# Performance work log

Hardware: AMD Instinct MI355X
Metric: run time of the kernel (lower is better)

## Reference

```python
import jax, jax.numpy as jnp
import numpy as np

B, S, HID = 2, 2048, 3072
H, HKV, D = 16, 8, 256
ROPE_THETA = 10000.0
NEG_INF = -1e9


def setup_inputs() -> dict:
    key = jax.random.key(0)
    ks = jax.random.split(key, 5)
    hidden_states = jax.random.normal(ks[0], (B, S, HID), jnp.float32)
    # rotary frequencies: complex freqs_cis = cos + i*sin, shape (B, S, D//2)
    inv_freq = 1.0 / (ROPE_THETA ** (np.arange(0, D, 2, dtype=np.float32) / D))
    ang = np.arange(S, dtype=np.float32)[:, None] * inv_freq[None, :]  # (S, D//2)
    cos = jnp.asarray(np.broadcast_to(np.cos(ang)[None], (B, S, D // 2)).copy())
    sin = jnp.asarray(np.broadcast_to(np.sin(ang)[None], (B, S, D // 2)).copy())
    causal = jnp.tril(jnp.ones((S, S), dtype=bool))
    mask = jnp.where(causal, 0.0, NEG_INF).astype(jnp.float32)[None, None]  # (1,1,S,S)
    wq = jax.random.normal(ks[1], (HID, H * D), jnp.float32) * 0.02
    wk = jax.random.normal(ks[2], (HID, HKV * D), jnp.float32) * 0.02
    wv = jax.random.normal(ks[3], (HID, HKV * D), jnp.float32) * 0.02
    wo = jax.random.normal(ks[4], (H * D, HID), jnp.float32) * 0.02
    return {"hidden_states": hidden_states, "cos": cos, "sin": sin, "mask": mask,
            "wq": wq, "wk": wk, "wv": wv, "wo": wo}


def _apply_rotary(x, cos, sin):
    # x: (B, S, Hx, D). Torch code forms complex pairs (x[..., :D/2], x[..., D/2:])
    # and multiplies by freqs_cis = cos + i*sin, then re-concats real||imag halves.
    half = x.shape[-1] // 2
    x1, x2 = x[..., :half], x[..., half:]
    c = cos[:, :, None, :]  # (B, S, 1, D/2)
    s = sin[:, :, None, :]
    return jnp.concatenate([x1 * c - x2 * s, x1 * s + x2 * c], axis=-1)


def reference(hidden_states, cos, sin, mask, wq, wk, wv, wo):
    b, s, _ = hidden_states.shape
    q = (hidden_states @ wq).reshape(b, s, H, D)
    k = (hidden_states @ wk).reshape(b, s, HKV, D)
    v = (hidden_states @ wv).reshape(b, s, HKV, D)
    q = _apply_rotary(q, cos, sin)
    k = _apply_rotary(k, cos, sin)
    # GQA: group query heads per kv head instead of materializing repeated K/V
    g = H // HKV
    qg = q.reshape(b, s, HKV, g, D)
    scaling = D ** (-0.5)
    scores = jnp.einsum('bskgd,btkd->bkgst', qg, k) * scaling  # (B,HKV,G,S,S)
    scores = scores + mask[:, :, None]  # broadcast (1,1,1,S,S)
    probs = jax.nn.softmax(scores, axis=-1)
    out = jnp.einsum('bkgst,btkd->bskgd', probs, v).reshape(b, s, H * D)
    return out @ wo
```

## Files before the change

### kernel.cpp

```cpp
#include <hip/hip_runtime.h>

typedef short bf16x8 __attribute__((ext_vector_type(8)));
typedef float f32x4 __attribute__((ext_vector_type(4)));

#define S_LEN 2048
#define NHQ 16
#define NKV 8
#define HD 256

__device__ __forceinline__ unsigned short f2bf(float f){
  unsigned u = __float_as_uint(f);
  unsigned r = (u + 0x7FFFu + ((u >> 16) & 1u)) >> 16;
  return (unsigned short)r;
}
__device__ __forceinline__ float bf2f(unsigned short h){
  return __uint_as_float(((unsigned)h) << 16);
}
__device__ __forceinline__ unsigned pack2(float a, float b){
  return (unsigned)f2bf(a) | ((unsigned)f2bf(b) << 16);
}

__global__ void k_conv(const float* __restrict__ in, unsigned short* __restrict__ out, int n){
  int i = (blockIdx.x * 256 + threadIdx.x) * 4;
  if (i < n){
    float4 v = *(const float4*)&in[i];
    ushort4 o;
    o.x = f2bf(v.x); o.y = f2bf(v.y); o.z = f2bf(v.z); o.w = f2bf(v.w);
    *(ushort4*)&out[i] = o;
  }
}

__global__ void k_tconv(const float* __restrict__ in, unsigned short* __restrict__ out, int R, int C){
  __shared__ float tile[32][33];
  int c0 = blockIdx.x * 32, r0 = blockIdx.y * 32;
  int tx = threadIdx.x, ty = threadIdx.y;
  for (int i = 0; i < 4; i++)
    tile[ty + i*8][tx] = in[(size_t)(r0 + ty + i*8) * C + c0 + tx];
  __syncthreads();
  for (int i = 0; i < 4; i++)
    out[(size_t)(c0 + ty + i*8) * R + r0 + tx] = f2bf(tile[tx][ty + i*8]);
}

__global__ void k_vtrans(const unsigned short* __restrict__ V, unsigned short* __restrict__ VT){
  __shared__ unsigned short tile[32][40];
  int s0 = blockIdx.x * 32, d0 = blockIdx.y * 32, bz = blockIdx.z;
  int b = bz >> 3, kv = bz & 7;
  int tx = threadIdx.x, ty = threadIdx.y;
  for (int i = 0; i < 4; i++)
    tile[ty + i*8][tx] = V[(size_t)(b * S_LEN + s0 + ty + i*8) * (NKV*HD) + kv*HD + d0 + tx];
  __syncthreads();
  for (int i = 0; i < 4; i++)
    VT[((size_t)(bz * HD + d0 + ty + i*8)) * S_LEN + s0 + tx] = tile[tx][ty + i*8];
}

__global__ void k_rope(unsigned short* buf, const float* __restrict__ cosb,
                       const float* __restrict__ sinb, int lgnh){
  int idx = blockIdx.x * 256 + threadIdx.x;
  int d = idx & 127;
  int h = (idx >> 7) & ((1 << lgnh) - 1);
  int t = idx >> (7 + lgnh);
  float c = cosb[t * 128 + d], s = sinb[t * 128 + d];
  size_t base = ((size_t)t << (lgnh + 8)) + ((size_t)h << 8) + d;
  float x1 = bf2f(buf[base]), x2 = bf2f(buf[base + 128]);
  buf[base]       = f2bf(x1 * c - x2 * s);
  buf[base + 128] = f2bf(x1 * s + x2 * c);
}

__global__ __launch_bounds__(256) void k_gemm_bt(const unsigned short* __restrict__ A,
    const unsigned short* __restrict__ Bt, void* __restrict__ Cp,
    int M, int N, int K, int out_bf16){
  __shared__ __align__(16) unsigned short smem[2 * 128 * 64];
  unsigned short* As = smem;
  unsigned short* Bs = smem + 128 * 64;
  int tid = threadIdx.x;
  int lane = tid & 63, wave = tid >> 6, quad = lane >> 4, l16 = lane & 15;
  int wm = wave >> 1, wn = wave & 1;
  int bm0 = blockIdx.y * 128, bn0 = blockIdx.x * 128;
  f32x4 acc[4][4] = {};
  for (int k0 = 0; k0 < K; k0 += 64){
    __syncthreads();
    for (int it = 0; it < 4; it++){
      int slot = it * 256 + tid;
      int row = slot >> 3, c = slot & 7;
      int pc = c ^ (row & 7);
      *(uint4*)&As[row * 64 + pc * 8] = *(const uint4*)&A[(size_t)(bm0 + row) * K + k0 + c * 8];
      *(uint4*)&Bs[row * 64 + pc * 8] = *(const uint4*)&Bt[(size_t)(bn0 + row) * K + k0 + c * 8];
    }
    __syncthreads();
    for (int ks = 0; ks < 2; ks++){
      bf16x8 af[4], bfr[4];
      for (int mt = 0; mt < 4; mt++){
        int row = wm * 64 + mt * 16 + l16;
        int pc = (ks * 4 + quad) ^ (row & 7);
        af[mt] = *(const bf16x8*)&As[row * 64 + pc * 8];
      }
      for (int nt = 0; nt < 4; nt++){
        int row = wn * 64 + nt * 16 + l16;
        int pc = (ks * 4 + quad) ^ (row & 7);
        bfr[nt] = *(const bf16x8*)&Bs[row * 64 + pc * 8];
      }
      for (int mt = 0; mt < 4; mt++)
        for (int nt = 0; nt < 4; nt++)
          acc[mt][nt] = __builtin_amdgcn_mfma_f32_16x16x32_bf16(af[mt], bfr[nt], acc[mt][nt], 0, 0, 0);
    }
  }
  float* Ct = (float*)smem;
  for (int p = 0; p < 2; p++){
    __syncthreads();
    if (wm == p){
      for (int mt = 0; mt < 4; mt++)
        for (int nt = 0; nt < 4; nt++)
          for (int r = 0; r < 4; r++)
            Ct[(mt * 16 + quad * 4 + r) * 128 + wn * 64 + nt * 16 + l16] = acc[mt][nt][r];
    }
    __syncthreads();
    if (out_bf16){
      unsigned short* O = (unsigned short*)Cp;
      for (int j = 0; j < 4; j++){
        int chunk = j * 256 + tid;
        int row = chunk >> 4, col = (chunk & 15) * 8;
        const float* src = &Ct[row * 128 + col];
        uint4 o;
        o.x = pack2(src[0], src[1]);
        o.y = pack2(src[2], src[3]);
        o.z = pack2(src[4], src[5]);
        o.w = pack2(src[6], src[7]);
        *(uint4*)&O[(size_t)(bm0 + p * 64 + row) * N + bn0 + col] = o;
      }
    } else {
      float* O = (float*)Cp;
      for (int j = 0; j < 8; j++){
        int chunk = j * 256 + tid;
        int row = chunk >> 5, col = (chunk & 31) * 4;
        *(float4*)&O[(size_t)(bm0 + p * 64 + row) * N + bn0 + col] = *(const float4*)&Ct[row * 128 + col];
      }
    }
  }
}

__global__ __launch_bounds__(256) void k_flash(const unsigned short* __restrict__ Q,
    const unsigned short* __restrict__ Kg, const unsigned short* __restrict__ VTg,
    unsigned short* __restrict__ Og){
  __shared__ __align__(16) unsigned short smem[32 * 264 + 256 * 40 + 4 * 16 * 40];
  unsigned short* Ks  = smem;
  unsigned short* VTs = smem + 32 * 264;
  unsigned short* Ps  = VTs + 256 * 40;
  int tid = threadIdx.x;
  int lane = tid & 63, wave = tid >> 6, quad = lane >> 4, l16 = lane & 15;
  int qt = blockIdx.x, hd_ = blockIdx.y;
  int b = hd_ >> 4, h = hd_ & 15, kv = h >> 1;

  bf16x8 qf[8];
  {
    size_t qoff = ((size_t)(b * S_LEN + qt * 64 + wave * 16 + l16)) * (NHQ * HD) + (size_t)h * HD;
    for (int ks = 0; ks < 8; ks++)
      qf[ks] = *(const bf16x8*)&Q[qoff + ks * 32 + quad * 8];
  }
  f32x4 acc[16] = {};
  float mrow[4], lrow[4];
  for (int r = 0; r < 4; r++){ mrow[r] = -1e30f; lrow[r] = 0.f; }
  int qmin = qt * 64 + wave * 16;
  int nkt = qt * 2 + 2;
  const float L2E = 1.4426950408889634f;
  const float scale = 0.0625f;

  for (int kt = 0; kt < nkt; kt++){
    __syncthreads();
    for (int it = 0; it < 4; it++){
      int slot = it * 256 + tid;
      int kr = slot >> 5, c = slot & 31;
      *(uint4*)&Ks[kr * 264 + c * 8] =
          *(const uint4*)&Kg[(size_t)(b * S_LEN + kt * 32 + kr) * (NKV*HD) + (size_t)kv * HD + c * 8];
      int dd = slot >> 2, c2 = slot & 3;
      *(uint4*)&VTs[dd * 40 + c2 * 8] =
          *(const uint4*)&VTg[((size_t)((b * NKV + kv) * HD + dd)) * S_LEN + kt * 32 + c2 * 8];
    }
    __syncthreads();
    if (kt * 32 > qmin + 15) continue;

    f32x4 sv[2] = {};
    for (int ks = 0; ks < 8; ks++){
      for (int nt = 0; nt < 2; nt++){
        bf16x8 kf = *(const bf16x8*)&Ks[(nt * 16 + l16) * 264 + ks * 32 + quad * 8];
        sv[nt] = __builtin_amdgcn_mfma_f32_16x16x32_bf16(qf[ks], kf, sv[nt], 0, 0, 0);
      }
    }
    float pv[2][4], tmax[4];
    for (int r = 0; r < 4; r++){
      int qr = qmin + quad * 4 + r;
      float mx = -1e30f;
      for (int nt = 0; nt < 2; nt++){
        int key = kt * 32 + nt * 16 + l16;
        float v = sv[nt][r] * scale;
        if (key > qr) v = -1e30f;
        pv[nt][r] = v;
        mx = fmaxf(mx, v);
      }
      tmax[r] = mx;
    }
    for (int off = 1; off < 16; off <<= 1)
      for (int r = 0; r < 4; r++)
        tmax[r] = fmaxf(tmax[r], __shfl_xor(tmax[r], off, 64));
    float alpha[4];
    for (int r = 0; r < 4; r++){
      float mn = fmaxf(mrow[r], tmax[r]);
      alpha[r] = exp2f((mrow[r] - mn) * L2E);
      mrow[r] = mn;
    }
    float pb[2][4], psum[4] = {0.f, 0.f, 0.f, 0.f};
    for (int nt = 0; nt < 2; nt++)
      for (int r = 0; r < 4; r++){
        float p = exp2f((pv[nt][r] - mrow[r]) * L2E);
        pb[nt][r] = p; psum[r] += p;
      }
    for (int off = 1; off < 16; off <<= 1)
      for (int r = 0; r < 4; r++)
        psum[r] += __shfl_xor(psum[r], off, 64);
    for (int r = 0; r < 4; r++) lrow[r] = lrow[r] * alpha[r] + psum[r];
    for (int i = 0; i < 16; i++)
      for (int r = 0; r < 4; r++) acc[i][r] *= alpha[r];
    int pbase = wave * 16 * 40;
    for (int nt = 0; nt < 2; nt++)
      for (int r = 0; r < 4; r++)
        Ps[pbase + (quad * 4 + r) * 40 + nt * 16 + l16] = f2bf(pb[nt][r]);
    bf16x8 pa = *(const bf16x8*)&Ps[pbase + l16 * 40 + quad * 8];
    for (int nt = 0; nt < 16; nt++){
      bf16x8 vf = *(const bf16x8*)&VTs[(nt * 16 + l16) * 40 + quad * 8];
      acc[nt] = __builtin_amdgcn_mfma_f32_16x16x32_bf16(pa, vf, acc[nt], 0, 0, 0);
    }
  }
  float inv[4];
  for (int r = 0; r < 4; r++) inv[r] = 1.0f / lrow[r];
  __syncthreads();
  unsigned short* Ot = smem + wave * 16 * 256;
  for (int nt = 0; nt < 16; nt++)
    for (int r = 0; r < 4; r++)
      Ot[(quad * 4 + r) * 256 + nt * 16 + l16] = f2bf(acc[nt][r] * inv[r]);
  size_t obase = ((size_t)(b * S_LEN + qt * 64 + wave * 16)) * (NHQ * HD) + (size_t)h * HD;
  for (int j = 0; j < 8; j++){
    int chunk = j * 64 + lane;
    int row = chunk >> 5, col = (chunk & 31) * 8;
    *(uint4*)&Og[obase + (size_t)row * (NHQ * HD) + col] = *(const uint4*)&Ot[row * 256 + col];
  }
}

extern "C" void kernel_launch(void* const* d_in, const int* in_sizes, int n_in,
                              void* d_out, int out_size, void* d_ws, size_t ws_size,
                              hipStream_t stream){
  const float* hid  = (const float*)d_in[0];
  const float* cosb = (const float*)d_in[1];
  const float* sinb = (const float*)d_in[2];
  const float* wq = (const float*)d_in[4];
  const float* wk = (const float*)d_in[5];
  const float* wv = (const float*)d_in[6];
  const float* wo = (const float*)d_in[7];

  char* ws = (char*)d_ws;
  size_t off = 0;
  auto alloc = [&](size_t bytes) -> void* {
    void* p = ws + off; off += (bytes + 255) & ~(size_t)255; return p;
  };
  unsigned short* Xbf = (unsigned short*)alloc(4096ull * 3072 * 2);
  unsigned short* WqT = (unsigned short*)alloc(4096ull * 3072 * 2);
  unsigned short* WkT = (unsigned short*)alloc(2048ull * 3072 * 2);
  unsigned short* WvT = (unsigned short*)alloc(2048ull * 3072 * 2);
  unsigned short* WoT = (unsigned short*)alloc(3072ull * 4096 * 2);
  unsigned short* Qb  = (unsigned short*)alloc(4096ull * 4096 * 2);
  unsigned short* Kb  = (unsigned short*)alloc(4096ull * 2048 * 2);
  unsigned short* Vb  = (unsigned short*)alloc(4096ull * 2048 * 2);
  unsigned short* VTb = (unsigned short*)alloc(4096ull * 2048 * 2);
  unsigned short* Ab  = (unsigned short*)alloc(4096ull * 4096 * 2);

  k_conv<<<12288, 256, 0, stream>>>(hid, Xbf, 4096 * 3072);
  k_tconv<<<dim3(128, 96), dim3(32, 8), 0, stream>>>(wq, WqT, 3072, 4096);
  k_tconv<<<dim3(64, 96),  dim3(32, 8), 0, stream>>>(wk, WkT, 3072, 2048);
  k_tconv<<<dim3(64, 96),  dim3(32, 8), 0, stream>>>(wv, WvT, 3072, 2048);
  k_tconv<<<dim3(96, 128), dim3(32, 8), 0, stream>>>(wo, WoT, 4096, 3072);
  k_gemm_bt<<<dim3(32, 32), 256, 0, stream>>>(Xbf, WqT, Qb, 4096, 4096, 3072, 1);
  k_gemm_bt<<<dim3(16, 32), 256, 0, stream>>>(Xbf, WkT, Kb, 4096, 2048, 3072, 1);
  k_gemm_bt<<<dim3(16, 32), 256, 0, stream>>>(Xbf, WvT, Vb, 4096, 2048, 3072, 1);
  k_rope<<<32768, 256, 0, stream>>>(Qb, cosb, sinb, 4);
  k_rope<<<16384, 256, 0, stream>>>(Kb, cosb, sinb, 3);
  k_vtrans<<<dim3(64, 8, 16), dim3(32, 8), 0, stream>>>(Vb, VTb);
  k_flash<<<dim3(32, 32), 256, 0, stream>>>(Qb, Kb, VTb, Ab);
  k_gemm_bt<<<dim3(24, 32), 256, 0, stream>>>(Ab, WoT, d_out, 4096, 3072, 4096, 0);
}
```

Before: 1.056 ms.

## Share K/V tiles across GQA heads in flash kernel, use direct-to-LDS loads in GEMM

```diff
diff --git a/kernel.cpp b/kernel.cpp
--- a/kernel.cpp
+++ b/kernel.cpp
@@ -18,6 +18,12 @@
 }
 __device__ __forceinline__ unsigned pack2(float a, float b){
   return (unsigned)f2bf(a) | ((unsigned)f2bf(b) << 16);
+}
+__device__ __forceinline__ void g2l16(const unsigned short* g, unsigned short* l){
+  __builtin_amdgcn_global_load_lds(
+      (const __attribute__((address_space(1))) unsigned int*)g,
+      (__attribute__((address_space(3))) unsigned int*)l,
+      16, 0, 0);
 }
 
 __global__ void k_conv(const float* __restrict__ in, unsigned short* __restrict__ out, int n){
@@ -76,15 +82,17 @@
   int lane = tid & 63, wave = tid >> 6, quad = lane >> 4, l16 = lane & 15;
   int wm = wave >> 1, wn = wave & 1;
   int bm0 = blockIdx.y * 128, bn0 = blockIdx.x * 128;
+  int lrow = lane >> 3;
+  int pc_s = lane & 7;
   f32x4 acc[4][4] = {};
   for (int k0 = 0; k0 < K; k0 += 64){
     __syncthreads();
-    for (int it = 0; it < 4; it++){
-      int slot = it * 256 + tid;
-      int row = slot >> 3, c = slot & 7;
-      int pc = c ^ (row & 7);
-      *(uint4*)&As[row * 64 + pc * 8] = *(const uint4*)&A[(size_t)(bm0 + row) * K + k0 + c * 8];
-      *(uint4*)&Bs[row * 64 + pc * 8] = *(const uint4*)&Bt[(size_t)(bn0 + row) * K + k0 + c * 8];
+    for (int i = 0; i < 4; i++){
+      int chunk = wave * 4 + i;
+      int row = chunk * 8 + lrow;
+      int c = pc_s ^ (row & 7);
+      g2l16(&A[(size_t)(bm0 + row) * K + k0 + c * 8], &As[chunk * 512]);
+      g2l16(&Bt[(size_t)(bn0 + row) * K + k0 + c * 8], &Bs[chunk * 512]);
     }
     __syncthreads();
     for (int ks = 0; ks < 2; ks++){
@@ -138,109 +146,145 @@
   }
 }
 
-__global__ __launch_bounds__(256) void k_flash(const unsigned short* __restrict__ Q,
+#define KS_STRIDE 296
+__global__ __launch_bounds__(256, 2) void k_flash(const unsigned short* __restrict__ Q,
     const unsigned short* __restrict__ Kg, const unsigned short* __restrict__ VTg,
     unsigned short* __restrict__ Og){
-  __shared__ __align__(16) unsigned short smem[32 * 264 + 256 * 40 + 4 * 16 * 40];
+  __shared__ __align__(16) unsigned short smem[32 * KS_STRIDE + 256 * 40 + 4 * 32 * 40];
   unsigned short* Ks  = smem;
-  unsigned short* VTs = smem + 32 * 264;
+  unsigned short* VTs = smem + 32 * KS_STRIDE;
   unsigned short* Ps  = VTs + 256 * 40;
   int tid = threadIdx.x;
   int lane = tid & 63, wave = tid >> 6, quad = lane >> 4, l16 = lane & 15;
-  int qt = blockIdx.x, hd_ = blockIdx.y;
-  int b = hd_ >> 4, h = hd_ & 15, kv = h >> 1;
-
-  bf16x8 qf[8];
-  {
-    size_t qoff = ((size_t)(b * S_LEN + qt * 64 + wave * 16 + l16)) * (NHQ * HD) + (size_t)h * HD;
+  int bkv = blockIdx.x;
+  int qt = 31 - (int)blockIdx.y;
+  int b = bkv >> 3, kv = bkv & 7;
+  int h = kv * 2 + (wave >> 1);
+  int qbase = qt * 64 + (wave & 1) * 32;
+
+  bf16x8 qf[2][8];
+  for (int f = 0; f < 2; f++){
+    size_t qoff = ((size_t)(b * S_LEN + qbase + f * 16 + l16)) * (NHQ * HD) + (size_t)h * HD;
     for (int ks = 0; ks < 8; ks++)
-      qf[ks] = *(const bf16x8*)&Q[qoff + ks * 32 + quad * 8];
-  }
-  f32x4 acc[16] = {};
-  float mrow[4], lrow[4];
-  for (int r = 0; r < 4; r++){ mrow[r] = -1e30f; lrow[r] = 0.f; }
-  int qmin = qt * 64 + wave * 16;
+      qf[f][ks] = *(const bf16x8*)&Q[qoff + ks * 32 + quad * 8];
+  }
+  f32x4 acc[32] = {};
+  float mrow[2][4], lrow[2][4];
+  for (int f = 0; f < 2; f++)
+    for (int r = 0; r < 4; r++){ mrow[f][r] = -1e30f; lrow[f][r] = 0.f; }
   int nkt = qt * 2 + 2;
   const float L2E = 1.4426950408889634f;
   const float scale = 0.0625f;
+  int pbase = wave * 32 * 40;
 
   for (int kt = 0; kt < nkt; kt++){
     __syncthreads();
     for (int it = 0; it < 4; it++){
       int slot = it * 256 + tid;
       int kr = slot >> 5, c = slot & 31;
-      *(uint4*)&Ks[kr * 264 + c * 8] =
+      *(uint4*)&Ks[kr * KS_STRIDE + c * 8] =
           *(const uint4*)&Kg[(size_t)(b * S_LEN + kt * 32 + kr) * (NKV*HD) + (size_t)kv * HD + c * 8];
       int dd = slot >> 2, c2 = slot & 3;
       *(uint4*)&VTs[dd * 40 + c2 * 8] =
           *(const uint4*)&VTg[((size_t)((b * NKV + kv) * HD + dd)) * S_LEN + kt * 32 + c2 * 8];
     }
     __syncthreads();
-    if (kt * 32 > qmin + 15) continue;
-
-    f32x4 sv[2] = {};
+    bool act0 = kt * 32 <= qbase + 15;
+    bool act1 = kt * 32 <= qbase + 31;
+    if (!act1) continue;
+
+    f32x4 sv[2][2] = {};
     for (int ks = 0; ks < 8; ks++){
       for (int nt = 0; nt < 2; nt++){
-        bf16x8 kf = *(const bf16x8*)&Ks[(nt * 16 + l16) * 264 + ks * 32 + quad * 8];
-        sv[nt] = __builtin_amdgcn_mfma_f32_16x16x32_bf16(qf[ks], kf, sv[nt], 0, 0, 0);
-      }
-    }
-    float pv[2][4], tmax[4];
-    for (int r = 0; r < 4; r++){
-      int qr = qmin + quad * 4 + r;
-      float mx = -1e30f;
-      for (int nt = 0; nt < 2; nt++){
-        int key = kt * 32 + nt * 16 + l16;
-        float v = sv[nt][r] * scale;
-        if (key > qr) v = -1e30f;
-        pv[nt][r] = v;
-        mx = fmaxf(mx, v);
-      }
-      tmax[r] = mx;
-    }
-    for (int off = 1; off < 16; off <<= 1)
+        bf16x8 kf = *(const bf16x8*)&Ks[(nt * 16 + l16) * KS_STRIDE + ks * 32 + quad * 8];
+        sv[0][nt] = __builtin_amdgcn_mfma_f32_16x16x32_bf16(qf[0][ks], kf, sv[0][nt], 0, 0, 0);
+        if (act0)
+          sv[1][nt] = __builtin_amdgcn_mfma_f32_16x16x32_bf16(qf[1][ks], kf, sv[1][nt], 0, 0, 0);
+      }
+    }
+
+    bf16x8 pa[2];
+    float inv_unused; (void)inv_unused;
+    for (int f = 0; f < 2; f++){
+      bool actf = (f == 0) ? act0 : act1;
+      if (!actf) continue;
+      f32x4* svf;
+      f32x4 svtmp[2];
+      if (f == 1 && !act0){
+        svtmp[0] = (f32x4){0,0,0,0}; svtmp[1] = (f32x4){0,0,0,0};
+        for (int ks = 0; ks < 8; ks++)
+          for (int nt = 0; nt < 2; nt++){
+            bf16x8 kf = *(const bf16x8*)&Ks[(nt * 16 + l16) * KS_STRIDE + ks * 32 + quad * 8];
+            svtmp[nt] = __builtin_amdgcn_mfma_f32_16x16x32_bf16(qf[1][ks], kf, svtmp[nt], 0, 0, 0);
+          }
+        svf = svtmp;
+      } else {
+        svf = sv[f];
+      }
+      int qminf = qbase + f * 16;
+      float pv[2][4], tmax[4];
+      for (int r = 0; r < 4; r++){
+        int qr = qminf + quad * 4 + r;
+        float mx = -1e30f;
+        for (int nt = 0; nt < 2; nt++){
+          int key = kt * 32 + nt * 16 + l16;
+          float v = svf[nt][r] * scale;
+          if (key > qr) v = -1e30f;
+          pv[nt][r] = v;
+          mx = fmaxf(mx, v);
+        }
+        tmax[r] = mx;
+      }
+      for (int off = 1; off < 16; off <<= 1)
+        for (int r = 0; r < 4; r++)
+          tmax[r] = fmaxf(tmax[r], __shfl_xor(tmax[r], off, 64));
+      float alpha[4];
+      for (int r = 0; r < 4; r++){
+        float mn = fmaxf(mrow[f][r], tmax[r]);
+        alpha[r] = exp2f((mrow[f][r] - mn) * L2E);
+        mrow[f][r] = mn;
+      }
+      float pb[2][4], psum[4] = {0.f, 0.f, 0.f, 0.f};
+      for (int nt = 0; nt < 2; nt++)
+        for (int r = 0; r < 4; r++){
+          float p = exp2f((pv[nt][r] - mrow[f][r]) * L2E);
+          pb[nt][r] = p; psum[r] += p;
+        }
+      for (int off = 1; off < 16; off <<= 1)
+        for (int r = 0; r < 4; r++)
+          psum[r] += __shfl_xor(psum[r], off, 64);
+      float amin = fminf(fminf(alpha[0], alpha[1]), fminf(alpha[2], alpha[3]));
+      for (int r = 0; r < 4; r++) lrow[f][r] = lrow[f][r] * alpha[r] + psum[r];
+      if (__any(amin < 1.0f)){
+        for (int dt = 0; dt < 16; dt++)
+          for (int r = 0; r < 4; r++) acc[f * 16 + dt][r] *= alpha[r];
+      }
+      for (int nt = 0; nt < 2; nt++)
+        for (int r = 0; r < 4; r++)
+          Ps[pbase + (f * 16 + quad * 4 + r) * 40 + nt * 16 + l16] = f2bf(pb[nt][r]);
+      pa[f] = *(const bf16x8*)&Ps[pbase + (f * 16 + l16) * 40 + quad * 8];
+    }
+    for (int dt = 0; dt < 16; dt++){
+      bf16x8 vf = *(const bf16x8*)&VTs[(dt * 16 + l16) * 40 + quad * 8];
+      if (act0) acc[dt]      = __builtin_amdgcn_mfma_f32_16x16x32_bf16(pa[0], vf, acc[dt], 0, 0, 0);
+      acc[16 + dt] = __builtin_amdgcn_mfma_f32_16x16x32_bf16(pa[1], vf, acc[16 + dt], 0, 0, 0);
+    }
+  }
+  float inv[2][4];
+  for (int f = 0; f < 2; f++)
+    for (int r = 0; r < 4; r++) inv[f][r] = 1.0f / lrow[f][r];
+  __syncthreads();
+  unsigned short* Ot = smem + wave * 4096;
+  for (int f = 0; f < 2; f++){
+    for (int dt = 0; dt < 16; dt++)
       for (int r = 0; r < 4; r++)
-        tmax[r] = fmaxf(tmax[r], __shfl_xor(tmax[r], off, 64));
-    float alpha[4];
-    for (int r = 0; r < 4; r++){
-      float mn = fmaxf(mrow[r], tmax[r]);
-      alpha[r] = exp2f((mrow[r] - mn) * L2E);
-      mrow[r] = mn;
-    }
-    float pb[2][4], psum[4] = {0.f, 0.f, 0.f, 0.f};
-    for (int nt = 0; nt < 2; nt++)
-      for (int r = 0; r < 4; r++){
-        float p = exp2f((pv[nt][r] - mrow[r]) * L2E);
-        pb[nt][r] = p; psum[r] += p;
-      }
-    for (int off = 1; off < 16; off <<= 1)
-      for (int r = 0; r < 4; r++)
-        psum[r] += __shfl_xor(psum[r], off, 64);
-    for (int r = 0; r < 4; r++) lrow[r] = lrow[r] * alpha[r] + psum[r];
-    for (int i = 0; i < 16; i++)
-      for (int r = 0; r < 4; r++) acc[i][r] *= alpha[r];
-    int pbase = wave * 16 * 40;
-    for (int nt = 0; nt < 2; nt++)
-      for (int r = 0; r < 4; r++)
-        Ps[pbase + (quad * 4 + r) * 40 + nt * 16 + l16] = f2bf(pb[nt][r]);
-    bf16x8 pa = *(const bf16x8*)&Ps[pbase + l16 * 40 + quad * 8];
-    for (int nt = 0; nt < 16; nt++){
-      bf16x8 vf = *(const bf16x8*)&VTs[(nt * 16 + l16) * 40 + quad * 8];
-      acc[nt] = __builtin_amdgcn_mfma_f32_16x16x32_bf16(pa, vf, acc[nt], 0, 0, 0);
-    }
-  }
-  float inv[4];
-  for (int r = 0; r < 4; r++) inv[r] = 1.0f / lrow[r];
-  __syncthreads();
-  unsigned short* Ot = smem + wave * 16 * 256;
-  for (int nt = 0; nt < 16; nt++)
-    for (int r = 0; r < 4; r++)
-      Ot[(quad * 4 + r) * 256 + nt * 16 + l16] = f2bf(acc[nt][r] * inv[r]);
-  size_t obase = ((size_t)(b * S_LEN + qt * 64 + wave * 16)) * (NHQ * HD) + (size_t)h * HD;
-  for (int j = 0; j < 8; j++){
-    int chunk = j * 64 + lane;
-    int row = chunk >> 5, col = (chunk & 31) * 8;
-    *(uint4*)&Og[obase + (size_t)row * (NHQ * HD) + col] = *(const uint4*)&Ot[row * 256 + col];
+        Ot[(quad * 4 + r) * 256 + dt * 16 + l16] = f2bf(acc[f * 16 + dt][r] * inv[f][r]);
+    size_t obase = ((size_t)(b * S_LEN + qbase + f * 16)) * (NHQ * HD) + (size_t)h * HD;
+    for (int j = 0; j < 8; j++){
+      int chunk = j * 64 + lane;
+      int row = chunk >> 5, col = (chunk & 31) * 8;
+      *(uint4*)&Og[obase + (size_t)row * (NHQ * HD) + col] = *(const uint4*)&Ot[row * 256 + col];
+    }
   }
 }
 
@@ -282,6 +326,6 @@
   k_rope<<<32768, 256, 0, stream>>>(Qb, cosb, sinb, 4);
   k_rope<<<16384, 256, 0, stream>>>(Kb, cosb, sinb, 3);
   k_vtrans<<<dim3(64, 8, 16), dim3(32, 8), 0, stream>>>(Vb, VTb);
-  k_flash<<<dim3(32, 32), 256, 0, stream>>>(Qb, Kb, VTb, Ab);
+  k_flash<<<dim3(16, 32), 256, 0, stream>>>(Qb, Kb, VTb, Ab);
   k_gemm_bt<<<dim3(24, 32), 256, 0, stream>>>(Ab, WoT, d_out, 4096, 3072, 4096, 0);
 }
```

New measurement: 1.181 ms. +11.8%, slower.
